# Kernel optimization log

Measured on AMD Instinct MI355X. Metric: run time of the kernel, lower is better.

## Reference

```python
import jax, jax.numpy as jnp
import numpy as np

N = 512          # number of ROI boxes
C = 1024         # detector box_head feature dim (in_feats)
HID_REPN = 256   # RePN hidden
HID = 256        # GAT hidden per head
HEADS = 4
NUM_CLASSES = 91
IMG_H, IMG_W = 800.0, 800.0
NEG_SLOPE = 0.2  # PyG GATConv default leaky relu slope


def setup_inputs() -> dict:
    key = jax.random.key(0)
    ks = jax.random.split(key, 12)
    s = 0.05
    feats = jax.random.normal(ks[0], (N, C), jnp.float32)
    # valid boxes: x1<x2, y1<y2, inside 800x800 image
    xy = jax.random.uniform(ks[1], (N, 2), jnp.float32, 0.0, 600.0)
    wh = jax.random.uniform(ks[2], (N, 2), jnp.float32, 10.0, 200.0)
    boxes = jnp.concatenate([xy, xy + wh], axis=1)
    # RelationProposalNetwork params (fc1: [hid, 2C+4], fc2: [1, hid])
    repn_w1 = jax.random.normal(ks[3], (HID_REPN, 2 * C + 4), jnp.float32) * s
    repn_b1 = jnp.zeros((HID_REPN,), jnp.float32)
    repn_w2 = jax.random.normal(ks[4], (1, HID_REPN), jnp.float32) * s
    repn_b2 = jnp.zeros((1,), jnp.float32)
    # AttentionalGCN: GATConv1 (in=C+4 -> HID, HEADS, concat), GATConv2 (HEADS*HID -> NUM_CLASSES, 1 head)
    gat1_w = jax.random.normal(ks[5], (C + 4, HEADS * HID), jnp.float32) * s
    gat1_asrc = jax.random.normal(ks[6], (HEADS, HID), jnp.float32) * s
    gat1_adst = jax.random.normal(ks[7], (HEADS, HID), jnp.float32) * s
    gat1_b = jnp.zeros((HEADS * HID,), jnp.float32)
    gat2_w = jax.random.normal(ks[8], (HEADS * HID, NUM_CLASSES), jnp.float32) * s
    gat2_asrc = jax.random.normal(ks[9], (1, NUM_CLASSES), jnp.float32) * s
    gat2_adst = jax.random.normal(ks[10], (1, NUM_CLASSES), jnp.float32) * s
    gat2_b = jnp.zeros((NUM_CLASSES,), jnp.float32)
    return dict(feats=feats, boxes=boxes,
                repn_w1=repn_w1, repn_b1=repn_b1, repn_w2=repn_w2, repn_b2=repn_b2,
                gat1_w=gat1_w, gat1_asrc=gat1_asrc, gat1_adst=gat1_adst, gat1_b=gat1_b,
                gat2_w=gat2_w, gat2_asrc=gat2_asrc, gat2_adst=gat2_adst, gat2_b=gat2_b,
                k=5)


def _gat_conv(x, src, dst, W, a_src, a_dst, bias, n, heads, out_c, concat_heads):
    # PyG GATConv: h = xW, e_uv = leakyrelu(a_src.h_u + a_dst.h_v), softmax over incoming
    # edges of target v, out_v = sum_u alpha_uv h_u (+ bias). Self-loops already in src/dst.
    h = (x @ W).reshape(n, heads, out_c)                       # [N,H,F]
    a_s = jnp.einsum('nhf,hf->nh', h, a_src)                   # [N,H]
    a_d = jnp.einsum('nhf,hf->nh', h, a_dst)
    e = jax.nn.leaky_relu(a_s[src] + a_d[dst], NEG_SLOPE)      # [E,H]
    m = jax.ops.segment_max(e, dst, num_segments=n)            # [N,H]
    m = jnp.where(jnp.isfinite(m), m, 0.0)
    ex = jnp.exp(e - m[dst])
    denom = jax.ops.segment_sum(ex, dst, num_segments=n)
    alpha = ex / (denom[dst] + 1e-16)                          # [E,H]
    out = jax.ops.segment_sum(alpha[:, :, None] * h[src], dst, num_segments=n)  # [N,H,F]
    out = out.reshape(n, heads * out_c) if concat_heads else out.mean(axis=1)
    return out + bias


def reference(feats, boxes, repn_w1, repn_b1, repn_w2, repn_b2,
              gat1_w, gat1_asrc, gat1_adst, gat1_b,
              gat2_w, gat2_asrc, gat2_adst, gat2_b, k):
    n, c = feats.shape
    # --- RelationProposalNetwork: fc1(cat[f_i, f_j, |b_i-b_j|]) without materializing [N,N,2C+4]
    wf1, wf2, wg = repn_w1[:, :c], repn_w1[:, c:2 * c], repn_w1[:, 2 * c:]
    p1 = feats @ wf1.T                                          # [N,hid]
    p2 = feats @ wf2.T                                          # [N,hid]
    geom_pair = jnp.abs(boxes[:, None, :] - boxes[None, :, :])  # [N,N,4]
    pg = jnp.einsum('ijd,hd->ijh', geom_pair, wg)               # [N,N,hid]
    h = jax.nn.relu(p1[:, None, :] + p2[None, :, :] + pg + repn_b1)
    rel = jnp.einsum('ijh,h->ij', h, repn_w2[0]) + repn_b2[0]   # [N,N] relation scores
    # --- kNN graph via topk (skip self at rank 0), as in _make_edge_index (N > k branch)
    _, idx = jax.lax.top_k(rel, k + 1)
    nbrs = idx[:, 1:]                                           # [N,k]
    src = jnp.repeat(jnp.arange(n), k)
    dst = nbrs.reshape(-1)
    loop = jnp.arange(n)                                        # PyG GATConv adds self-loops
    src = jnp.concatenate([src, loop])
    dst = jnp.concatenate([dst, loop])
    # --- node features: [roi_feats, normalized box geometry]
    scale = jnp.array([IMG_W, IMG_H, IMG_W, IMG_H], jnp.float32)
    nb = boxes / scale
    geom = jnp.stack([nb[:, 0], nb[:, 1], nb[:, 2] - nb[:, 0], nb[:, 3] - nb[:, 1]], axis=1)
    x = jnp.concatenate([feats, geom], axis=1)                  # [N, C+4]
    # --- AttentionalGCN: relu(GAT1) -> GAT2
    h1 = jax.nn.relu(_gat_conv(x, src, dst, gat1_w, gat1_asrc, gat1_adst, gat1_b, n, HEADS, HID, True))
    logits = _gat_conv(h1, src, dst, gat2_w, gat2_asrc, gat2_adst, gat2_b, n, 1, NUM_CLASSES, True)
    probs = jax.nn.softmax(logits, axis=1)                      # per-node class probs
    return logits, probs, rel
```

## Files before the change

kernel.cpp:

```cpp
#include <hip/hip_runtime.h>

#define NCLS 91
#define W1_LD 2052

typedef __attribute__((ext_vector_type(8))) short short8;
typedef __attribute__((ext_vector_type(4))) float f32x4;

__device__ inline ushort bf16_rne(float x) {
    unsigned u = __float_as_uint(x);
    return (ushort)((u + 0x7fffu + ((u >> 16) & 1u)) >> 16);
}

__global__ __launch_bounds__(128) void k_p12(const float* __restrict__ feats,
                                             const float* __restrict__ w1f,
                                             float* __restrict__ pp) {
    int r0 = blockIdx.x * 64, i0 = blockIdx.y * 32, z = blockIdx.z;
    int tid = threadIdx.x, tx = tid & 15, ty = tid >> 4;
    __shared__ float As[64 * 32];
    __shared__ float Bs[64 * 64];
    float* pout = pp + z * 262144;
    int ai = tid & 31, akq = (tid >> 5) * 16;
    int br = tid & 63, bkq = (tid >> 6) * 32;
    const float* abase = feats + (i0 + ai) * 1024 + z * 256 + akq;
    int rg = r0 + br;
    const float* bbase = w1f + (rg < 256 ? rg * W1_LD : (rg - 256) * W1_LD + 1024)
                       + z * 256 + bkq;
    float4 av[4], bv[8];
#pragma unroll
    for (int s = 0; s < 4; ++s) av[s] = *(const float4*)(abase + 4 * s);
#pragma unroll
    for (int s = 0; s < 8; ++s) bv[s] = *(const float4*)(bbase + 4 * s);
    float acc[4][4] = {};
    for (int kt = 0; kt < 4; ++kt) {
#pragma unroll
        for (int s = 0; s < 4; ++s) {
            int k = akq + 4 * s;
            As[(k + 0) * 32 + ai] = av[s].x; As[(k + 1) * 32 + ai] = av[s].y;
            As[(k + 2) * 32 + ai] = av[s].z; As[(k + 3) * 32 + ai] = av[s].w;
        }
#pragma unroll
        for (int s = 0; s < 8; ++s) {
            int k = bkq + 4 * s;
            Bs[(k + 0) * 64 + br] = bv[s].x; Bs[(k + 1) * 64 + br] = bv[s].y;
            Bs[(k + 2) * 64 + br] = bv[s].z; Bs[(k + 3) * 64 + br] = bv[s].w;
        }
        __syncthreads();
        if (kt + 1 < 4) {
#pragma unroll
            for (int s = 0; s < 4; ++s) av[s] = *(const float4*)(abase + (kt + 1) * 64 + 4 * s);
#pragma unroll
            for (int s = 0; s < 8; ++s) bv[s] = *(const float4*)(bbase + (kt + 1) * 64 + 4 * s);
        }
#pragma unroll
        for (int k = 0; k < 64; ++k) {
            float4 a4 = *(const float4*)(As + k * 32 + ty * 4);
            float4 b4 = *(const float4*)(Bs + k * 64 + tx * 4);
            acc[0][0] = fmaf(a4.x, b4.x, acc[0][0]); acc[0][1] = fmaf(a4.x, b4.y, acc[0][1]);
            acc[0][2] = fmaf(a4.x, b4.z, acc[0][2]); acc[0][3] = fmaf(a4.x, b4.w, acc[0][3]);
            acc[1][0] = fmaf(a4.y, b4.x, acc[1][0]); acc[1][1] = fmaf(a4.y, b4.y, acc[1][1]);
            acc[1][2] = fmaf(a4.y, b4.z, acc[1][2]); acc[1][3] = fmaf(a4.y, b4.w, acc[1][3]);
            acc[2][0] = fmaf(a4.z, b4.x, acc[2][0]); acc[2][1] = fmaf(a4.z, b4.y, acc[2][1]);
            acc[2][2] = fmaf(a4.z, b4.z, acc[2][2]); acc[2][3] = fmaf(a4.z, b4.w, acc[2][3]);
            acc[3][0] = fmaf(a4.w, b4.x, acc[3][0]); acc[3][1] = fmaf(a4.w, b4.y, acc[3][1]);
            acc[3][2] = fmaf(a4.w, b4.z, acc[3][2]); acc[3][3] = fmaf(a4.w, b4.w, acc[3][3]);
        }
        __syncthreads();
    }
#pragma unroll
    for (int ii = 0; ii < 4; ++ii)
        *(float4*)(pout + (i0 + ty * 4 + ii) * 512 + r0 + tx * 4) =
            make_float4(acc[ii][0], acc[ii][1], acc[ii][2], acc[ii][3]);
}

__global__ __launch_bounds__(256) void k_rel(const float* __restrict__ pp,
                                             const float* __restrict__ w1f,
                                             const float* __restrict__ b1f,
                                             const float* __restrict__ w2f,
                                             const float* __restrict__ boxesf,
                                             float* __restrict__ r0,
                                             float* __restrict__ r1) {
    int j0 = blockIdx.x * 64, i0 = blockIdx.y * 16, z = blockIdx.z;
    int tid = threadIdx.x, tx = tid & 63, ty = tid >> 6;
    __shared__ float As1[32 * 17];
    __shared__ float Bs[32 * 64];
    __shared__ float Awg[32 * 4];
    __shared__ float Aw2[32];
    float4 bj = *(const float4*)(boxesf + (j0 + tx) * 4);
    float g[4][4];
#pragma unroll
    for (int s = 0; s < 4; ++s) {
        float4 bi = *(const float4*)(boxesf + (i0 + ty * 4 + s) * 4);
        g[s][0] = fabsf(bi.x - bj.x); g[s][1] = fabsf(bi.y - bj.y);
        g[s][2] = fabsf(bi.z - bj.z); g[s][3] = fabsf(bi.w - bj.w);
    }
    float acc[4] = {0.f, 0.f, 0.f, 0.f};
    int ali = tid & 15, alh = (tid >> 4) * 4;
    int blj = tid & 63, blh = (tid >> 6) * 8;
    for (int c4 = 0; c4 < 4; ++c4) {
        int hb = (z * 4 + c4) * 32;
        if (tid < 128) {
            int base = (i0 + ali) * 512 + hb + alh;
            float4 v0 = *(const float4*)(pp + base);
            float4 v1 = *(const float4*)(pp + 262144 + base);
            float4 v2 = *(const float4*)(pp + 524288 + base);
            float4 v3 = *(const float4*)(pp + 786432 + base);
            float4 b  = *(const float4*)(b1f + hb + alh);
            As1[(alh + 0) * 17 + ali] = v0.x + v1.x + v2.x + v3.x + b.x;
            As1[(alh + 1) * 17 + ali] = v0.y + v1.y + v2.y + v3.y + b.y;
            As1[(alh + 2) * 17 + ali] = v0.z + v1.z + v2.z + v3.z + b.z;
            As1[(alh + 3) * 17 + ali] = v0.w + v1.w + v2.w + v3.w + b.w;
        }
#pragma unroll
        for (int s = 0; s < 2; ++s) {
            int h = blh + 4 * s;
            int base = (j0 + blj) * 512 + 256 + hb + h;
            float4 u0 = *(const float4*)(pp + base);
            float4 u1 = *(const float4*)(pp + 262144 + base);
            float4 u2 = *(const float4*)(pp + 524288 + base);
            float4 u3 = *(const float4*)(pp + 786432 + base);
            Bs[(h + 0) * 64 + blj] = u0.x + u1.x + u2.x + u3.x;
            Bs[(h + 1) * 64 + blj] = u0.y + u1.y + u2.y + u3.y;
            Bs[(h + 2) * 64 + blj] = u0.z + u1.z + u2.z + u3.z;
            Bs[(h + 3) * 64 + blj] = u0.w + u1.w + u2.w + u3.w;
        }
        if (tid < 32) {
            int hg = hb + tid;
            *(float4*)(Awg + tid * 4) = *(const float4*)(w1f + hg * W1_LD + 2048);
            Aw2[tid] = w2f[hg];
        }
        __syncthreads();
#pragma unroll
        for (int hh = 0; hh < 32; ++hh) {
            float4 wg = *(const float4*)(Awg + hh * 4);
            float w2v = Aw2[hh];
            float p2v = Bs[hh * 64 + tx];
            float s0 = As1[hh * 17 + ty * 4 + 0];
            float s1 = As1[hh * 17 + ty * 4 + 1];
            float s2 = As1[hh * 17 + ty * 4 + 2];
            float s3 = As1[hh * 17 + ty * 4 + 3];
            float t0 = s0 + p2v;
            t0 = fmaf(g[0][0], wg.x, t0); t0 = fmaf(g[0][1], wg.y, t0);
            t0 = fmaf(g[0][2], wg.z, t0); t0 = fmaf(g[0][3], wg.w, t0);
            acc[0] = fmaf(w2v, fmaxf(t0, 0.f), acc[0]);
            float t1 = s1 + p2v;
            t1 = fmaf(g[1][0], wg.x, t1); t1 = fmaf(g[1][1], wg.y, t1);
            t1 = fmaf(g[1][2], wg.z, t1); t1 = fmaf(g[1][3], wg.w, t1);
            acc[1] = fmaf(w2v, fmaxf(t1, 0.f), acc[1]);
            float t2 = s2 + p2v;
            t2 = fmaf(g[2][0], wg.x, t2); t2 = fmaf(g[2][1], wg.y, t2);
            t2 = fmaf(g[2][2], wg.z, t2); t2 = fmaf(g[2][3], wg.w, t2);
            acc[2] = fmaf(w2v, fmaxf(t2, 0.f), acc[2]);
            float t3 = s3 + p2v;
            t3 = fmaf(g[3][0], wg.x, t3); t3 = fmaf(g[3][1], wg.y, t3);
            t3 = fmaf(g[3][2], wg.z, t3); t3 = fmaf(g[3][3], wg.w, t3);
            acc[3] = fmaf(w2v, fmaxf(t3, 0.f), acc[3]);
        }
        __syncthreads();
    }
    float* po = z ? r1 : r0;
#pragma unroll
    for (int s = 0; s < 4; ++s)
        po[(i0 + ty * 4 + s) * 512 + j0 + tx] = acc[s];
}

__global__ void k_topk(const float* __restrict__ r0, const float* __restrict__ r1,
                       const float* __restrict__ b2f, const int* __restrict__ kp,
                       int* __restrict__ nbrs, int* __restrict__ count,
                       float* __restrict__ rel_out) {
    int i = blockIdx.x, lane = threadIdx.x;
    int k = *kp;
    float b2v = b2f[0];
    float v[8]; int ids[8];
    for (int q = 0; q < 8; ++q) {
        int j = lane + 64 * q;
        float val = r0[i * 512 + j] + r1[i * 512 + j] + b2v;
        rel_out[i * 512 + j] = val;
        v[q] = val;
        ids[q] = j;
    }
    for (int pick = 0; pick < k + 1; ++pick) {
        float bv = -INFINITY; int bidx = 1 << 30;
        for (int q = 0; q < 8; ++q)
            if (v[q] > bv || (v[q] == bv && ids[q] < bidx)) { bv = v[q]; bidx = ids[q]; }
        for (int off = 32; off > 0; off >>= 1) {
            float ov = __shfl_down(bv, off);
            int oi = __shfl_down(bidx, off);
            if (ov > bv || (ov == bv && oi < bidx)) { bv = ov; bidx = oi; }
        }
        bv = __shfl(bv, 0); bidx = __shfl(bidx, 0);
        if (pick >= 1 && lane == 0) {
            nbrs[i * 8 + (pick - 1)] = bidx;
            atomicAdd(&count[bidx], 1);
        }
        for (int q = 0; q < 8; ++q) if (ids[q] == bidx) v[q] = -INFINITY;
    }
    if (lane == 0) atomicAdd(&count[i], 1);
}

__global__ void k_scan(const int* __restrict__ count, int* __restrict__ offs) {
    __shared__ int s[512];
    int t = threadIdx.x;
    s[t] = count[t];
    __syncthreads();
    for (int off = 1; off < 512; off <<= 1) {
        int v = (t >= off) ? s[t - off] : 0;
        __syncthreads();
        s[t] += v;
        __syncthreads();
    }
    offs[t + 1] = s[t];
    if (t == 0) offs[0] = 0;
}

__global__ void k_fill(const int* __restrict__ nbrs, const int* __restrict__ kp,
                       const int* __restrict__ offs, int* __restrict__ cursor,
                       int* __restrict__ inlist) {
    int i = blockIdx.x * blockDim.x + threadIdx.x;
    if (i >= 512) return;
    int k = *kp;
    for (int q = 0; q < k; ++q) {
        int d = nbrs[i * 8 + q] & 511;
        int pos = atomicAdd(&cursor[d], 1);
        inlist[offs[d] + pos] = i;
    }
    int pos = atomicAdd(&cursor[i], 1);
    inlist[offs[i] + pos] = i;
}

__global__ __launch_bounds__(256) void k_conv(const float* __restrict__ feats,
                                              const float* __restrict__ Wg,
                                              ushort* __restrict__ Afh,
                                              ushort* __restrict__ Afl,
                                              ushort* __restrict__ Bfh,
                                              ushort* __restrict__ Bfl,
                                              int* __restrict__ zero_ints) {
    int b = blockIdx.x, t = threadIdx.x;
    if (b < 4) zero_ints[b * 256 + t] = 0;
    int lane = t & 63;
    float x[8];
    size_t off;
    if (b < 256) {
        int g = b * 256 + t;
        int q = g >> 6;
        int it = q & 31, kt = q >> 5;
        int row = it * 16 + (lane & 15);
        int col0 = kt * 32 + (lane >> 4) * 8;
        const float* src = feats + row * 1024 + col0;
        float4 u0 = *(const float4*)(src);
        float4 u1 = *(const float4*)(src + 4);
        x[0] = u0.x; x[1] = u0.y; x[2] = u0.z; x[3] = u0.w;
        x[4] = u1.x; x[5] = u1.y; x[6] = u1.z; x[7] = u1.w;
        off = ((size_t)(kt * 32 + it) * 64 + lane) * 8;
    } else {
        int g = (b - 256) * 256 + t;
        int q = g >> 6;
        int nt = q & 63, kt = q >> 6;
        int col = nt * 16 + (lane & 15);
        int row0 = kt * 32 + (lane >> 4) * 8;
#pragma unroll
        for (int e = 0; e < 8; ++e) x[e] = Wg[(row0 + e) * 1024 + col];
        off = ((size_t)(kt * 64 + nt) * 64 + lane) * 8;
        Afh = Bfh; Afl = Bfl;
    }
    uint uh[4], ul[4];
#pragma unroll
    for (int p = 0; p < 4; ++p) {
        ushort h0 = bf16_rne(x[2 * p]);
        ushort h1 = bf16_rne(x[2 * p + 1]);
        float f0 = __uint_as_float((unsigned)h0 << 16);
        float f1 = __uint_as_float((unsigned)h1 << 16);
        ushort l0 = bf16_rne(x[2 * p] - f0);
        ushort l1 = bf16_rne(x[2 * p + 1] - f1);
        uh[p] = (uint)h0 | ((uint)h1 << 16);
        ul[p] = (uint)l0 | ((uint)l1 << 16);
    }
    *(uint4*)(Afh + off) = make_uint4(uh[0], uh[1], uh[2], uh[3]);
    *(uint4*)(Afl + off) = make_uint4(ul[0], ul[1], ul[2], ul[3]);
}

__global__ __launch_bounds__(256) void k_mm1(const ushort* __restrict__ Afh,
                                             const ushort* __restrict__ Afl,
                                             const ushort* __restrict__ Bfh,
                                             const ushort* __restrict__ Bfl,
                                             float* __restrict__ P) {
    int nt0 = blockIdx.x * 4, it0 = blockIdx.y * 4, z = blockIdx.z;
    int t = threadIdx.x, lane = t & 63, w = t >> 6;
    int wr = w >> 1, wc = w & 1, sub = w;
    __shared__ uint4 buf[2][4][4][64];
    const uint4* gAh = (const uint4*)Afh;
    const uint4* gAl = (const uint4*)Afl;
    const uint4* gBh = (const uint4*)Bfh;
    const uint4* gBl = (const uint4*)Bfl;
    f32x4 acc[2][2];
    f32x4 zero = {0.f, 0.f, 0.f, 0.f};
    acc[0][0] = zero; acc[0][1] = zero; acc[1][0] = zero; acc[1][1] = zero;
    int ktg = z * 8;
    uint4 rah = gAh[(ktg * 32 + it0 + sub) * 64 + lane];
    uint4 ral = gAl[(ktg * 32 + it0 + sub) * 64 + lane];
    uint4 rbh = gBh[(ktg * 64 + nt0 + sub) * 64 + lane];
    uint4 rbl = gBl[(ktg * 64 + nt0 + sub) * 64 + lane];
    for (int kk = 0; kk < 8; ++kk) {
        int cur = kk & 1;
        buf[cur][0][sub][lane] = rah;
        buf[cur][1][sub][lane] = ral;
        buf[cur][2][sub][lane] = rbh;
        buf[cur][3][sub][lane] = rbl;
        __syncthreads();
        if (kk < 7) {
            int kn = ktg + kk + 1;
            rah = gAh[(kn * 32 + it0 + sub) * 64 + lane];
            ral = gAl[(kn * 32 + it0 + sub) * 64 + lane];
            rbh = gBh[(kn * 64 + nt0 + sub) * 64 + lane];
            rbl = gBl[(kn * 64 + nt0 + sub) * 64 + lane];
        }
        short8 ah[2], al[2], bh[2], bl[2];
#pragma unroll
        for (int i = 0; i < 2; ++i) {
            ah[i] = *(const short8*)&buf[cur][0][2 * wr + i][lane];
            al[i] = *(const short8*)&buf[cur][1][2 * wr + i][lane];
            bh[i] = *(const short8*)&buf[cur][2][2 * wc + i][lane];
            bl[i] = *(const short8*)&buf[cur][3][2 * wc + i][lane];
        }
#pragma unroll
        for (int i = 0; i < 2; ++i)
#pragma unroll
            for (int j = 0; j < 2; ++j) {
                acc[i][j] = __builtin_amdgcn_mfma_f32_16x16x32_bf16(ah[i], bh[j], acc[i][j], 0, 0, 0);
                acc[i][j] = __builtin_amdgcn_mfma_f32_16x16x32_bf16(ah[i], bl[j], acc[i][j], 0, 0, 0);
                acc[i][j] = __builtin_amdgcn_mfma_f32_16x16x32_bf16(al[i], bh[j], acc[i][j], 0, 0, 0);
            }
        __syncthreads();
    }
    float* outp = P + z * 524288;
#pragma unroll
    for (int i = 0; i < 2; ++i)
#pragma unroll
        for (int j = 0; j < 2; ++j) {
            int rbase = (it0 + 2 * wr + i) * 16 + (lane >> 4) * 4;
            int c = (nt0 + 2 * wc + j) * 16 + (lane & 15);
#pragma unroll
            for (int r = 0; r < 4; ++r)
                outp[(size_t)(rbase + r) * 1024 + c] = acc[i][j][r];
        }
}

__global__ __launch_bounds__(256) void k_gat1ep(const float* __restrict__ P,
                                                const float* __restrict__ boxesf,
                                                const float* __restrict__ Wg,
                                                const float* __restrict__ asrcf,
                                                const float* __restrict__ adstf,
                                                float* __restrict__ hX,
                                                float* __restrict__ a_s1,
                                                float* __restrict__ a_d1) {
    int i = blockIdx.x, t = threadIdx.x;
    const float* P0 = P;
    const float* P1 = P + 524288;
    const float* P2 = P + 1048576;
    const float* P3 = P + 1572864;
    float4 bx = *(const float4*)(boxesf + i * 4);
    float g0 = bx.x / 800.f, g1 = bx.y / 800.f;
    float g2 = bx.z / 800.f - g0, g3 = bx.w / 800.f - g1;
    float ps[4], pd[4];
#pragma unroll
    for (int q = 0; q < 4; ++q) {
        int c = q * 256 + t;
        float v = P0[i * 1024 + c] + P1[i * 1024 + c] + P2[i * 1024 + c] + P3[i * 1024 + c];
        v = fmaf(g0, Wg[1024 * 1024 + c], v);
        v = fmaf(g1, Wg[1025 * 1024 + c], v);
        v = fmaf(g2, Wg[1026 * 1024 + c], v);
        v = fmaf(g3, Wg[1027 * 1024 + c], v);
        hX[i * 1024 + c] = v;
        ps[q] = v * asrcf[c];
        pd[q] = v * adstf[c];
    }
    __shared__ float rs[4][4], rd[4][4];
    int wid = t >> 6;
#pragma unroll
    for (int off = 32; off > 0; off >>= 1) {
#pragma unroll
        for (int q = 0; q < 4; ++q) {
            ps[q] += __shfl_down(ps[q], off);
            pd[q] += __shfl_down(pd[q], off);
        }
    }
    if ((t & 63) == 0) {
#pragma unroll
        for (int q = 0; q < 4; ++q) { rs[wid][q] = ps[q]; rd[wid][q] = pd[q]; }
    }
    __syncthreads();
    if (t < 4)
        a_s1[i * 4 + t] = rs[0][t] + rs[1][t] + rs[2][t] + rs[3][t];
    else if (t < 8) {
        int q = t - 4;
        a_d1[i * 4 + q] = rd[0][q] + rd[1][q] + rd[2][q] + rd[3][q];
    }
}

__global__ void k_aggr1(const float* __restrict__ hX,
                        const float* __restrict__ a_s, const float* __restrict__ a_d,
                        const int* __restrict__ offs, const int* __restrict__ inlist,
                        const float* __restrict__ bias,
                        float* __restrict__ h1) {
    int n = blockIdx.x, t = threadIdx.x;
    int beg = offs[n], deg = offs[n + 1] - beg;
    if (deg > 513) deg = 513;
    __shared__ int srcs[520];
    __shared__ float alpha[520][4];
    __shared__ float sm[4];
    for (int e = t; e < deg; e += 256) srcs[e] = inlist[beg + e] & 511;
    __syncthreads();
    for (int idx = t; idx < deg * 4; idx += 256) {
        int e = idx >> 2, q = idx & 3;
        float sc = a_s[srcs[e] * 4 + q] + a_d[n * 4 + q];
        alpha[e][q] = (sc >= 0.f) ? sc : 0.2f * sc;
    }
    __syncthreads();
    if (t < 4) {
        float m = -INFINITY;
        for (int e = 0; e < deg; ++e) m = fmaxf(m, alpha[e][t]);
        if (!isfinite(m)) m = 0.f;
        float s = 0.f;
        for (int e = 0; e < deg; ++e) { float ex = expf(alpha[e][t] - m); alpha[e][t] = ex; s += ex; }
        sm[t] = s + 1e-16f;
    }
    __syncthreads();
    for (int idx = t; idx < deg * 4; idx += 256) {
        int e = idx >> 2, q = idx & 3;
        alpha[e][q] /= sm[q];
    }
    __syncthreads();
    for (int q = 0; q < 4; ++q) {
        float acc = 0.f;
        for (int e = 0; e < deg; ++e) acc += alpha[e][q] * hX[srcs[e] * 1024 + q * 256 + t];
        h1[n * 1024 + q * 256 + t] = fmaxf(acc + bias[q * 256 + t], 0.f);
    }
}

__global__ __launch_bounds__(256) void k_gat2(const float* __restrict__ h1,
                                              const float* __restrict__ Wf,
                                              const float* __restrict__ asrcf,
                                              const float* __restrict__ adstf,
                                              float* __restrict__ h2,
                                              float* __restrict__ a_s2,
                                              float* __restrict__ a_d2) {
    int n = blockIdx.x, t = threadIdx.x;
    __shared__ float xs[1024];
    __shared__ float hbuf[NCLS];
    __shared__ float sred[256], dred[256];
    for (int c = t; c < 1024; c += 256) xs[c] = h1[n * 1024 + c];
    __syncthreads();
    int cls = t & 127, kh = t >> 7;
    float acc = 0.f;
    if (cls < NCLS) {
        const float* wp = Wf + (kh * 512) * NCLS + cls;
        const float* xp = xs + kh * 512;
        float a0 = 0.f, a1 = 0.f, a2 = 0.f, a3 = 0.f;
        for (int c = 0; c < 512; c += 4) {
            a0 = fmaf(xp[c + 0], wp[(c + 0) * NCLS], a0);
            a1 = fmaf(xp[c + 1], wp[(c + 1) * NCLS], a1);
            a2 = fmaf(xp[c + 2], wp[(c + 2) * NCLS], a2);
            a3 = fmaf(xp[c + 3], wp[(c + 3) * NCLS], a3);
        }
        acc = (a0 + a1) + (a2 + a3);
    }
    if (kh == 0 && cls < NCLS) hbuf[cls] = acc;
    __syncthreads();
    float tot = 0.f;
    int act = (kh == 1 && cls < NCLS);
    if (act) { tot = acc + hbuf[cls]; h2[n * NCLS + cls] = tot; }
    sred[t] = act ? tot * asrcf[cls] : 0.f;
    dred[t] = act ? tot * adstf[cls] : 0.f;
    __syncthreads();
    for (int s = 128; s > 0; s >>= 1) {
        if (t < s) { sred[t] += sred[t + s]; dred[t] += dred[t + s]; }
        __syncthreads();
    }
    if (t == 0) { a_s2[n] = sred[0]; a_d2[n] = dred[0]; }
}

__global__ void k_aggr2(const float* __restrict__ h2,
                        const float* __restrict__ a_s2, const float* __restrict__ a_d2,
                        const int* __restrict__ offs, const int* __restrict__ inlist,
                        const float* __restrict__ bias,
                        float* __restrict__ logits_out,
                        float* __restrict__ probs_out) {
    int n = blockIdx.x, t = threadIdx.x;
    int beg = offs[n], deg = offs[n + 1] - beg;
    if (deg > 513) deg = 513;
    __shared__ int srcs[520];
    __shared__ float alpha[520];
    __shared__ float red[128];
    __shared__ float smden;
    for (int e = t; e < deg; e += 128) {
        int s = inlist[beg + e] & 511;
        srcs[e] = s;
        float sc = a_s2[s] + a_d2[n];
        alpha[e] = (sc >= 0.f) ? sc : 0.2f * sc;
    }
    __syncthreads();
    if (t == 0) {
        float m = -INFINITY;
        for (int e = 0; e < deg; ++e) m = fmaxf(m, alpha[e]);
        if (!isfinite(m)) m = 0.f;
        float s = 0.f;
        for (int e = 0; e < deg; ++e) { float ex = expf(alpha[e] - m); alpha[e] = ex; s += ex; }
        smden = s + 1e-16f;
    }
    __syncthreads();
    float logit = 0.f;
    if (t < NCLS) {
        float acc = 0.f;
        for (int e = 0; e < deg; ++e) acc += alpha[e] * h2[srcs[e] * NCLS + t];
        logit = acc / smden + bias[t];
        logits_out[n * NCLS + t] = logit;
    }
    red[t] = (t < NCLS) ? logit : -INFINITY; __syncthreads();
    for (int s = 64; s > 0; s >>= 1) { if (t < s) red[t] = fmaxf(red[t], red[t + s]); __syncthreads(); }
    float mx = red[0];
    __syncthreads();
    float ex = (t < NCLS) ? expf(logit - mx) : 0.f;
    red[t] = ex; __syncthreads();
    for (int s = 64; s > 0; s >>= 1) { if (t < s) red[t] += red[t + s]; __syncthreads(); }
    float inv = 1.f / red[0];
    if (t < NCLS) probs_out[n * NCLS + t] = ex * inv;
}

extern "C" void kernel_launch(void* const* d_in, const int* in_sizes, int n_in,
                              void* d_out, int out_size, void* d_ws, size_t ws_size,
                              hipStream_t stream) {
    const float* feats   = (const float*)d_in[0];
    const float* boxes   = (const float*)d_in[1];
    const float* repn_w1 = (const float*)d_in[2];
    const float* repn_b1 = (const float*)d_in[3];
    const float* repn_w2 = (const float*)d_in[4];
    const float* repn_b2 = (const float*)d_in[5];
    const float* gat1_w    = (const float*)d_in[6];
    const float* gat1_asrc = (const float*)d_in[7];
    const float* gat1_adst = (const float*)d_in[8];
    const float* gat1_b    = (const float*)d_in[9];
    const float* gat2_w    = (const float*)d_in[10];
    const float* gat2_asrc = (const float*)d_in[11];
    const float* gat2_adst = (const float*)d_in[12];
    const float* gat2_b    = (const float*)d_in[13];
    const int* kp = (const int*)d_in[14];

    float* out = (float*)d_out;
    float* logits_out = out;
    float* probs_out  = out + 512 * NCLS;
    float* rel_out    = out + 2 * 512 * NCLS;

    float* wsf   = (float*)d_ws;
    float* pp    = wsf;
    float* prel1 = wsf + 1048576;
    float* P     = wsf + 1310720;
    float* hX    = P;
    float* h1    = P + 524288;
    ushort* Afh  = (ushort*)(wsf + 3407872);
    ushort* Afl  = (ushort*)(wsf + 3670016);
    ushort* Bfh  = (ushort*)(wsf + 3932160);
    ushort* Bfl  = (ushort*)(wsf + 4456448);
    float* h2    = wsf + 4980736;
    float* a_s2  = wsf + 5027840;
    float* a_d2  = wsf + 5028352;
    float* a_s1  = wsf + 5028864;
    float* a_d1  = wsf + 5030912;
    int* ib      = (int*)(wsf + 5032960);
    int* count   = ib;
    int* cursor  = ib + 512;
    int* nbrs    = ib + 1024;
    int* offs    = ib + 5120;
    int* inlist  = ib + 5640;

    k_conv<<<dim3(768), dim3(256), 0, stream>>>(feats, gat1_w, Afh, Afl, Bfh, Bfl, ib);
    k_p12<<<dim3(8, 16, 4), dim3(128), 0, stream>>>(feats, repn_w1, pp);
    k_rel<<<dim3(8, 32, 2), dim3(256), 0, stream>>>(pp, repn_w1, repn_b1, repn_w2,
                                                    boxes, rel_out, prel1);
    k_topk<<<dim3(512), dim3(64), 0, stream>>>(rel_out, prel1, repn_b2, kp,
                                               nbrs, count, rel_out);
    k_scan<<<dim3(1), dim3(512), 0, stream>>>(count, offs);
    k_fill<<<dim3(2), dim3(256), 0, stream>>>(nbrs, kp, offs, cursor, inlist);
    k_mm1<<<dim3(16, 8, 4), dim3(256), 0, stream>>>(Afh, Afl, Bfh, Bfl, P);
    k_gat1ep<<<dim3(512), dim3(256), 0, stream>>>(P, boxes, gat1_w, gat1_asrc,
                                                  gat1_adst, hX, a_s1, a_d1);
    k_aggr1<<<dim3(512), dim3(256), 0, stream>>>(hX, a_s1, a_d1, offs, inlist, gat1_b, h1);
    k_gat2<<<dim3(512), dim3(256), 0, stream>>>(h1, gat2_w, gat2_asrc, gat2_adst,
                                                h2, a_s2, a_d2);
    k_aggr2<<<dim3(512), dim3(128), 0, stream>>>(h2, a_s2, a_d2, offs, inlist, gat2_b,
                                                 logits_out, probs_out);
}
```

Baseline: 196.6 us.

## Double split-K in RePN GEMM and rel kernel, fuse scan and fill

The RePN projection GEMM now uses 8-way split-K instead of 4, so twice as many blocks launch with half the K per block. The relation kernel reduces 8 partials and splits the hidden dimension 4 ways, writing 3 extra partial maps that top-k sums. The scan and neighbour-fill kernels merge into one single-block kernel that uses shared-memory cursors, which saves a launch and a global cursor buffer. The cost is more partial-sum memory traffic and a reworked workspace layout.

```diff
diff --git a/kernel.cpp b/kernel.cpp
--- a/kernel.cpp
+++ b/kernel.cpp
@@ -21,17 +21,17 @@
     float* pout = pp + z * 262144;
     int ai = tid & 31, akq = (tid >> 5) * 16;
     int br = tid & 63, bkq = (tid >> 6) * 32;
-    const float* abase = feats + (i0 + ai) * 1024 + z * 256 + akq;
+    const float* abase = feats + (i0 + ai) * 1024 + z * 128 + akq;
     int rg = r0 + br;
     const float* bbase = w1f + (rg < 256 ? rg * W1_LD : (rg - 256) * W1_LD + 1024)
-                       + z * 256 + bkq;
+                       + z * 128 + bkq;
     float4 av[4], bv[8];
 #pragma unroll
     for (int s = 0; s < 4; ++s) av[s] = *(const float4*)(abase + 4 * s);
 #pragma unroll
     for (int s = 0; s < 8; ++s) bv[s] = *(const float4*)(bbase + 4 * s);
     float acc[4][4] = {};
-    for (int kt = 0; kt < 4; ++kt) {
+    for (int kt = 0; kt < 2; ++kt) {
 #pragma unroll
         for (int s = 0; s < 4; ++s) {
             int k = akq + 4 * s;
@@ -45,11 +45,11 @@
             Bs[(k + 2) * 64 + br] = bv[s].z; Bs[(k + 3) * 64 + br] = bv[s].w;
         }
         __syncthreads();
-        if (kt + 1 < 4) {
-#pragma unroll
-            for (int s = 0; s < 4; ++s) av[s] = *(const float4*)(abase + (kt + 1) * 64 + 4 * s);
-#pragma unroll
-            for (int s = 0; s < 8; ++s) bv[s] = *(const float4*)(bbase + (kt + 1) * 64 + 4 * s);
+        if (kt + 1 < 2) {
+#pragma unroll
+            for (int s = 0; s < 4; ++s) av[s] = *(const float4*)(abase + 64 + 4 * s);
+#pragma unroll
+            for (int s = 0; s < 8; ++s) bv[s] = *(const float4*)(bbase + 64 + 4 * s);
         }
 #pragma unroll
         for (int k = 0; k < 64; ++k) {
@@ -78,7 +78,7 @@
                                              const float* __restrict__ w2f,
                                              const float* __restrict__ boxesf,
                                              float* __restrict__ r0,
-                                             float* __restrict__ r1) {
+                                             float* __restrict__ prel) {
     int j0 = blockIdx.x * 64, i0 = blockIdx.y * 16, z = blockIdx.z;
     int tid = threadIdx.x, tx = tid & 63, ty = tid >> 6;
     __shared__ float As1[32 * 17];
@@ -96,32 +96,35 @@
     float acc[4] = {0.f, 0.f, 0.f, 0.f};
     int ali = tid & 15, alh = (tid >> 4) * 4;
     int blj = tid & 63, blh = (tid >> 6) * 8;
-    for (int c4 = 0; c4 < 4; ++c4) {
-        int hb = (z * 4 + c4) * 32;
+    for (int c4 = 0; c4 < 2; ++c4) {
+        int hb = (z * 2 + c4) * 32;
         if (tid < 128) {
             int base = (i0 + ali) * 512 + hb + alh;
-            float4 v0 = *(const float4*)(pp + base);
-            float4 v1 = *(const float4*)(pp + 262144 + base);
-            float4 v2 = *(const float4*)(pp + 524288 + base);
-            float4 v3 = *(const float4*)(pp + 786432 + base);
-            float4 b  = *(const float4*)(b1f + hb + alh);
-            As1[(alh + 0) * 17 + ali] = v0.x + v1.x + v2.x + v3.x + b.x;
-            As1[(alh + 1) * 17 + ali] = v0.y + v1.y + v2.y + v3.y + b.y;
-            As1[(alh + 2) * 17 + ali] = v0.z + v1.z + v2.z + v3.z + b.z;
-            As1[(alh + 3) * 17 + ali] = v0.w + v1.w + v2.w + v3.w + b.w;
+            float4 a4 = *(const float4*)(b1f + hb + alh);
+#pragma unroll
+            for (int p = 0; p < 8; ++p) {
+                float4 v = *(const float4*)(pp + p * 262144 + base);
+                a4.x += v.x; a4.y += v.y; a4.z += v.z; a4.w += v.w;
+            }
+            As1[(alh + 0) * 17 + ali] = a4.x;
+            As1[(alh + 1) * 17 + ali] = a4.y;
+            As1[(alh + 2) * 17 + ali] = a4.z;
+            As1[(alh + 3) * 17 + ali] = a4.w;
         }
 #pragma unroll
         for (int s = 0; s < 2; ++s) {
             int h = blh + 4 * s;
             int base = (j0 + blj) * 512 + 256 + hb + h;
-            float4 u0 = *(const float4*)(pp + base);
-            float4 u1 = *(const float4*)(pp + 262144 + base);
-            float4 u2 = *(const float4*)(pp + 524288 + base);
-            float4 u3 = *(const float4*)(pp + 786432 + base);
-            Bs[(h + 0) * 64 + blj] = u0.x + u1.x + u2.x + u3.x;
-            Bs[(h + 1) * 64 + blj] = u0.y + u1.y + u2.y + u3.y;
-            Bs[(h + 2) * 64 + blj] = u0.z + u1.z + u2.z + u3.z;
-            Bs[(h + 3) * 64 + blj] = u0.w + u1.w + u2.w + u3.w;
+            float4 u4 = make_float4(0.f, 0.f, 0.f, 0.f);
+#pragma unroll
+            for (int p = 0; p < 8; ++p) {
+                float4 v = *(const float4*)(pp + p * 262144 + base);
+                u4.x += v.x; u4.y += v.y; u4.z += v.z; u4.w += v.w;
+            }
+            Bs[(h + 0) * 64 + blj] = u4.x;
+            Bs[(h + 1) * 64 + blj] = u4.y;
+            Bs[(h + 2) * 64 + blj] = u4.z;
+            Bs[(h + 3) * 64 + blj] = u4.w;
         }
         if (tid < 32) {
             int hg = hb + tid;
@@ -157,13 +160,13 @@
         }
         __syncthreads();
     }
-    float* po = z ? r1 : r0;
+    float* po = (z == 0) ? r0 : (prel + (z - 1) * 262144);
 #pragma unroll
     for (int s = 0; s < 4; ++s)
         po[(i0 + ty * 4 + s) * 512 + j0 + tx] = acc[s];
 }
 
-__global__ void k_topk(const float* __restrict__ r0, const float* __restrict__ r1,
+__global__ void k_topk(const float* __restrict__ r0, const float* __restrict__ prel,
                        const float* __restrict__ b2f, const int* __restrict__ kp,
                        int* __restrict__ nbrs, int* __restrict__ count,
                        float* __restrict__ rel_out) {
@@ -173,7 +176,8 @@
     float v[8]; int ids[8];
     for (int q = 0; q < 8; ++q) {
         int j = lane + 64 * q;
-        float val = r0[i * 512 + j] + r1[i * 512 + j] + b2v;
+        float val = r0[i * 512 + j] + prel[i * 512 + j]
+                  + prel[262144 + i * 512 + j] + prel[524288 + i * 512 + j] + b2v;
         rel_out[i * 512 + j] = val;
         v[q] = val;
         ids[q] = j;
@@ -197,10 +201,15 @@
     if (lane == 0) atomicAdd(&count[i], 1);
 }
 
-__global__ void k_scan(const int* __restrict__ count, int* __restrict__ offs) {
+__global__ void k_scanfill(const int* __restrict__ count, const int* __restrict__ nbrs,
+                           const int* __restrict__ kp,
+                           int* __restrict__ offs, int* __restrict__ inlist) {
     __shared__ int s[512];
+    __shared__ int excl[512];
+    __shared__ int cur[512];
     int t = threadIdx.x;
-    s[t] = count[t];
+    int c = count[t];
+    s[t] = c; cur[t] = 0;
     __syncthreads();
     for (int off = 1; off < 512; off <<= 1) {
         int v = (t >= off) ? s[t - off] : 0;
@@ -210,21 +219,16 @@
     }
     offs[t + 1] = s[t];
     if (t == 0) offs[0] = 0;
-}
-
-__global__ void k_fill(const int* __restrict__ nbrs, const int* __restrict__ kp,
-                       const int* __restrict__ offs, int* __restrict__ cursor,
-                       int* __restrict__ inlist) {
-    int i = blockIdx.x * blockDim.x + threadIdx.x;
-    if (i >= 512) return;
+    excl[t] = s[t] - c;
+    __syncthreads();
     int k = *kp;
     for (int q = 0; q < k; ++q) {
-        int d = nbrs[i * 8 + q] & 511;
-        int pos = atomicAdd(&cursor[d], 1);
-        inlist[offs[d] + pos] = i;
-    }
-    int pos = atomicAdd(&cursor[i], 1);
-    inlist[offs[i] + pos] = i;
+        int d = nbrs[t * 8 + q] & 511;
+        int pos = atomicAdd(&cur[d], 1);
+        inlist[excl[d] + pos] = t;
+    }
+    int pos = atomicAdd(&cur[t], 1);
+    inlist[excl[t] + pos] = t;
 }
 
 __global__ __launch_bounds__(256) void k_conv(const float* __restrict__ feats,
@@ -235,7 +239,7 @@
                                               ushort* __restrict__ Bfl,
                                               int* __restrict__ zero_ints) {
     int b = blockIdx.x, t = threadIdx.x;
-    if (b < 4) zero_ints[b * 256 + t] = 0;
+    if (b < 2) zero_ints[b * 256 + t] = 0;
     int lane = t & 63;
     float x[8];
     size_t off;
@@ -551,34 +555,32 @@
 
     float* wsf   = (float*)d_ws;
     float* pp    = wsf;
-    float* prel1 = wsf + 1048576;
-    float* P     = wsf + 1310720;
+    float* P     = wsf;
     float* hX    = P;
     float* h1    = P + 524288;
-    ushort* Afh  = (ushort*)(wsf + 3407872);
-    ushort* Afl  = (ushort*)(wsf + 3670016);
-    ushort* Bfh  = (ushort*)(wsf + 3932160);
-    ushort* Bfl  = (ushort*)(wsf + 4456448);
-    float* h2    = wsf + 4980736;
-    float* a_s2  = wsf + 5027840;
-    float* a_d2  = wsf + 5028352;
-    float* a_s1  = wsf + 5028864;
-    float* a_d1  = wsf + 5030912;
-    int* ib      = (int*)(wsf + 5032960);
+    float* prel  = wsf + 2097152;
+    ushort* Afh  = (ushort*)(wsf + 2883584);
+    ushort* Afl  = (ushort*)(wsf + 3145728);
+    ushort* Bfh  = (ushort*)(wsf + 3407872);
+    ushort* Bfl  = (ushort*)(wsf + 3932160);
+    float* h2    = wsf + 4456448;
+    float* a_s2  = wsf + 4503552;
+    float* a_d2  = wsf + 4504064;
+    float* a_s1  = wsf + 4504576;
+    float* a_d1  = wsf + 4506624;
+    int* ib      = (int*)(wsf + 4508672);
     int* count   = ib;
-    int* cursor  = ib + 512;
     int* nbrs    = ib + 1024;
     int* offs    = ib + 5120;
     int* inlist  = ib + 5640;
 
     k_conv<<<dim3(768), dim3(256), 0, stream>>>(feats, gat1_w, Afh, Afl, Bfh, Bfl, ib);
-    k_p12<<<dim3(8, 16, 4), dim3(128), 0, stream>>>(feats, repn_w1, pp);
-    k_rel<<<dim3(8, 32, 2), dim3(256), 0, stream>>>(pp, repn_w1, repn_b1, repn_w2,
-                                                    boxes, rel_out, prel1);
-    k_topk<<<dim3(512), dim3(64), 0, stream>>>(rel_out, prel1, repn_b2, kp,
+    k_p12<<<dim3(8, 16, 8), dim3(128), 0, stream>>>(feats, repn_w1, pp);
+    k_rel<<<dim3(8, 32, 4), dim3(256), 0, stream>>>(pp, repn_w1, repn_b1, repn_w2,
+                                                    boxes, rel_out, prel);
+    k_topk<<<dim3(512), dim3(64), 0, stream>>>(rel_out, prel, repn_b2, kp,
                                                nbrs, count, rel_out);
-    k_scan<<<dim3(1), dim3(512), 0, stream>>>(count, offs);
-    k_fill<<<dim3(2), dim3(256), 0, stream>>>(nbrs, kp, offs, cursor, inlist);
+    k_scanfill<<<dim3(1), dim3(512), 0, stream>>>(count, nbrs, kp, offs, inlist);
     k_mm1<<<dim3(16, 8, 4), dim3(256), 0, stream>>>(Afh, Afl, Bfh, Bfl, P);
     k_gat1ep<<<dim3(512), dim3(256), 0, stream>>>(P, boxes, gat1_w, gat1_asrc,
                                                   gat1_adst, hX, a_s1, a_d1);
```

New measurement: 204.1 us. 1.04x slower.
